# Kernel optimization log

Hardware: AMD Instinct MI355X
Metric: run time of the kernel (lower is better)

Reference implementation:

```python
import jax, jax.numpy as jnp
import numpy as np
import math

B, L, D, P = 2, 2048, 256, 32

def _lin_init(key, fan_in, shape):
    return jax.random.normal(key, shape, dtype=jnp.float32) / np.float32(math.sqrt(fan_in))

def setup_inputs() -> dict:
    key = jax.random.key(0)
    ks = jax.random.split(key, 16)
    return {
        "x": jax.random.normal(ks[0], (B, L, D), dtype=jnp.float32),
        "pos_phases": jax.random.normal(ks[1], (L, P), dtype=jnp.float32) * np.float32(math.pi),
        "w_pos_value": _lin_init(ks[2], D, (D, D)), "b_pos_value": jnp.zeros((D,), jnp.float32),
        "w_key": _lin_init(ks[3], D, (D, P)), "b_key": jnp.zeros((P,), jnp.float32),
        "w_kv": _lin_init(ks[4], D, (D, D)), "b_kv": jnp.zeros((D,), jnp.float32),
        "w_vg1": _lin_init(ks[5], 2 * D, (2 * D, D)), "b_vg1": jnp.zeros((D,), jnp.float32),
        "w_vg2": _lin_init(ks[6], D, (D, 1)), "b_vg2": jnp.zeros((1,), jnp.float32),
        "w_bg1": _lin_init(ks[7], D, (D, D // 2)), "b_bg1": jnp.zeros((D // 2,), jnp.float32),
        "w_bg2": _lin_init(ks[8], D // 2, (D // 2, 2)), "b_bg2": jnp.zeros((2,), jnp.float32),
        "ln_r_g": jnp.ones((D,), jnp.float32), "ln_r_b": jnp.zeros((D,), jnp.float32),
        "w_r1": _lin_init(ks[9], D, (D, 2 * D)), "b_r1": jnp.zeros((2 * D,), jnp.float32),
        "w_r2": _lin_init(ks[10], 2 * D, (2 * D, D)), "b_r2": jnp.zeros((D,), jnp.float32),
        "ln_o_g": jnp.ones((D,), jnp.float32), "ln_o_b": jnp.zeros((D,), jnp.float32),
        "w_out": _lin_init(ks[11], D, (D, D)), "b_out": jnp.zeros((D,), jnp.float32),
    }

def _ln(z, g, b, eps=1e-5):
    mu = z.mean(-1, keepdims=True)
    var = ((z - mu) ** 2).mean(-1, keepdims=True)
    return (z - mu) * jax.lax.rsqrt(var + eps) * g + b

def _shift1(z):
    # torch.roll(shifts=1, dims=1) then zero first position == shift right with zero pad
    return jnp.concatenate([jnp.zeros_like(z[:, :1]), z[:, :-1]], axis=1)

def reference(x, pos_phases, w_pos_value, b_pos_value, w_key, b_key, w_kv, b_kv,
              w_vg1, b_vg1, w_vg2, b_vg2, w_bg1, b_bg1, w_bg2, b_bg2,
              ln_r_g, ln_r_b, w_r1, b_r1, w_r2, b_r2, ln_o_g, ln_o_b, w_out, b_out):
    Bv, Lv, Dv = x.shape
    Pv = pos_phases.shape[1]
    inv_sqrt_p = np.float32(1.0 / math.sqrt(Pv))

    # --- positional memory ---
    pos_phasors = jnp.exp(1j * pos_phases)                      # (L,P) complex64
    pos_values = (x @ w_pos_value + b_pos_value).astype(jnp.complex64)  # (B,L,D)
    pos_bound = pos_phasors[None, :, :, None] * pos_values[:, :, None, :]  # (B,L,P,D)
    pos_memory = jnp.cumsum(pos_bound, axis=1)
    pos_query = jnp.exp(-1j * pos_phases)                       # (L,P)
    pos_retrieved = (pos_memory * pos_query[None, :, :, None]).sum(axis=2).real * inv_sqrt_p

    # --- content-based KV memory ---
    key_phases = jnp.tanh(x @ w_key + b_key) * np.float32(math.pi)  # (B,L,P)
    key_phasors = jnp.exp(1j * key_phases)
    kv_values = (x @ w_kv + b_kv).astype(jnp.complex64)         # (B,L,D)

    x_shifted = _shift1(x)
    gate_input = jnp.concatenate([x, x_shifted], axis=-1)       # (B,L,2D)
    h = jax.nn.gelu(gate_input @ w_vg1 + b_vg1, approximate=False)
    value_gates = jax.nn.sigmoid(h @ w_vg2 + b_vg2)             # (B,L,1)

    key_phasors_shifted = _shift1(key_phasors)                  # (B,L,P)
    kv_bound = (key_phasors_shifted[..., None] * kv_values[:, :, None, :]) \
               * value_gates[:, :, :, None].astype(jnp.complex64)  # (B,L,P,D)
    kv_memory = jnp.cumsum(kv_bound, axis=1)
    gate_cumsum = jnp.maximum(jnp.cumsum(value_gates, axis=1), 1.0)  # (B,L,1)
    kv_query = jnp.exp(-1j * key_phases)                        # (B,L,P)
    kv_retrieved = (kv_memory * kv_query[..., None]).sum(axis=2).real
    kv_retrieved = kv_retrieved / (jnp.sqrt(gate_cumsum) * np.float32(math.sqrt(Pv)))

    # --- blend, refine, output ---
    bg_h = jax.nn.gelu(x @ w_bg1 + b_bg1, approximate=False)
    blend = jax.nn.softmax(bg_h @ w_bg2 + b_bg2, axis=-1)       # (B,L,2)
    blended = blend[..., 0:1] * pos_retrieved + blend[..., 1:2] * kv_retrieved

    refined = jax.nn.gelu(_ln(blended, ln_r_g, ln_r_b) @ w_r1 + b_r1, approximate=False) @ w_r2 + b_r2
    return x + (_ln(refined, ln_o_g, ln_o_b) @ w_out + b_out)
```

## Files before the change

kernel.cpp:

```cpp
#include <hip/hip_runtime.h>
#include <math.h>

#define B_ 2
#define L_ 2048
#define D_ 256
#define P_ 32
#define NC_ 64
#define CL_ 32

#define INV_SQRT_P 0.17677669529663687f
#define PI_F 3.14159265358979323846f

typedef __attribute__((ext_vector_type(8))) short bf16x8;
typedef __attribute__((ext_vector_type(4))) float f32x4;

__device__ __forceinline__ float gelu_exact(float x){
    return 0.5f * x * (1.0f + erff(x * 0.70710678118654752f));
}

__device__ __forceinline__ unsigned short f2bf(float f){
    unsigned int u = __float_as_uint(f);
    u += 0x7FFFu + ((u >> 16) & 1u);
    return (unsigned short)(u >> 16);
}

__global__ __launch_bounds__(256) void k_prep(
    const float* __restrict__ pos_phases,
    const float* __restrict__ w_pv, const float* __restrict__ w_kv,
    const float* __restrict__ w_vg1, const float* __restrict__ w_bg1,
    const float* __restrict__ w_r1, const float* __restrict__ w_r2,
    const float* __restrict__ w_out, const float* __restrict__ w_key,
    unsigned short* __restrict__ wq,
    float* __restrict__ cpos, float* __restrict__ spos)
{
    int id = blockIdx.x * 256 + threadIdx.x;
    if (id < 630784){
        const float* src; int N; int local;
        if (id < 65536)       { src = w_pv;  N = 256; local = id; }
        else if (id < 131072) { src = w_kv;  N = 256; local = id - 65536; }
        else if (id < 262144) { src = w_vg1; N = 256; local = id - 131072; }
        else if (id < 294912) { src = w_bg1; N = 128; local = id - 262144; }
        else if (id < 425984) { src = w_r1;  N = 512; local = id - 294912; }
        else if (id < 557056) { src = w_r2;  N = 256; local = id - 425984; }
        else if (id < 622592) { src = w_out; N = 256; local = id - 557056; }
        else                  { src = w_key; N = 32;  local = id - 622592; }
        int j = local & 7, lane = (local >> 3) & 63, tile = local >> 9;
        int NT = N >> 4;
        int nt = tile % NT, kt = tile / NT;
        int row = kt * 32 + ((lane >> 4) << 3) + j;
        int col = nt * 16 + (lane & 15);
        wq[id] = f2bf(src[(size_t)row * N + col]);
    } else {
        int idx = id - 630784;
        float s, c;
        sincosf(pos_phases[idx], &s, &c);
        cpos[idx] = c;
        spos[idx] = s;
    }
}

__global__ __launch_bounds__(512) void k_proj(
    const float* __restrict__ x,
    const unsigned short* __restrict__ wq,
    const float* __restrict__ b_pv, const float* __restrict__ b_kv,
    const float* __restrict__ b_vg1,
    const float* __restrict__ w_vg2, const float* __restrict__ b_vg2,
    const float* __restrict__ b_bg1,
    const float* __restrict__ w_bg2, const float* __restrict__ b_bg2,
    const float* __restrict__ b_key,
    float* __restrict__ pv, float* __restrict__ kvv,
    float* __restrict__ ck, float* __restrict__ sk,
    float* __restrict__ vg, float* __restrict__ blend0, float* __restrict__ blend1)
{
    __shared__ float hbuf[16][257];
    __shared__ float bhbuf[16][129];
    __shared__ float kph[16][33];
    __shared__ float red[16][17], red2[16][17], red3[16][17];

    const int i = threadIdx.x;
    const int lane = i & 63, w = i >> 6;
    const int b = blockIdx.x >> 7, lt = blockIdx.x & 127, l0 = lt * 16;
    const int g = lane >> 4, c = lane & 15;

    bf16x8 xa[8], xs[8];
    {
        int row  = l0 + (lane & 15);
        int rowp = row - 1;
        const float* xr = x + (size_t)(b * L_ + row) * D_ + ((lane >> 4) << 3);
        #pragma unroll
        for (int kt = 0; kt < 8; ++kt){
            float4 a0 = *(const float4*)(xr + kt * 32);
            float4 a1 = *(const float4*)(xr + kt * 32 + 4);
            bf16x8 v;
            v[0] = (short)f2bf(a0.x); v[1] = (short)f2bf(a0.y);
            v[2] = (short)f2bf(a0.z); v[3] = (short)f2bf(a0.w);
            v[4] = (short)f2bf(a1.x); v[5] = (short)f2bf(a1.y);
            v[6] = (short)f2bf(a1.z); v[7] = (short)f2bf(a1.w);
            xa[kt] = v;
        }
        if (rowp >= 0){
            const float* xp = x + (size_t)(b * L_ + rowp) * D_ + ((lane >> 4) << 3);
            #pragma unroll
            for (int kt = 0; kt < 8; ++kt){
                float4 a0 = *(const float4*)(xp + kt * 32);
                float4 a1 = *(const float4*)(xp + kt * 32 + 4);
                bf16x8 v;
                v[0] = (short)f2bf(a0.x); v[1] = (short)f2bf(a0.y);
                v[2] = (short)f2bf(a0.z); v[3] = (short)f2bf(a0.w);
                v[4] = (short)f2bf(a1.x); v[5] = (short)f2bf(a1.y);
                v[6] = (short)f2bf(a1.z); v[7] = (short)f2bf(a1.w);
                xs[kt] = v;
            }
        } else {
            #pragma unroll
            for (int kt = 0; kt < 8; ++kt){
                bf16x8 v;
                #pragma unroll
                for (int j = 0; j < 8; ++j) v[j] = 0;
                xs[kt] = v;
            }
        }
    }

    const unsigned short* wpv  = wq;
    const unsigned short* wkv  = wq + 65536;
    const unsigned short* wvg1 = wq + 131072;
    const unsigned short* wbg1 = wq + 262144;
    const unsigned short* wkey = wq + 622592;

    for (int jb = w; jb < 58; jb += 8){
        f32x4 acc = {0.f, 0.f, 0.f, 0.f};
        if (jb < 2){
            int nt = jb;
            #pragma unroll
            for (int kt = 0; kt < 8; ++kt){
                bf16x8 bf = *(const bf16x8*)(wkey + (kt * 2 + nt) * 512 + lane * 8);
                acc = __builtin_amdgcn_mfma_f32_16x16x32_bf16(xa[kt], bf, acc, 0, 0, 0);
            }
            float bb = b_key[nt * 16 + c];
            #pragma unroll
            for (int r = 0; r < 4; ++r)
                kph[4 * g + r][nt * 16 + c] = acc[r] + bb;
        } else if (jb < 18){
            int nt = jb - 2;
            #pragma unroll
            for (int kt = 0; kt < 8; ++kt){
                bf16x8 bf = *(const bf16x8*)(wpv + (kt * 16 + nt) * 512 + lane * 8);
                acc = __builtin_amdgcn_mfma_f32_16x16x32_bf16(xa[kt], bf, acc, 0, 0, 0);
            }
            float bb = b_pv[nt * 16 + c];
            #pragma unroll
            for (int r = 0; r < 4; ++r)
                pv[(size_t)(b * L_ + l0 + 4 * g + r) * D_ + nt * 16 + c] = acc[r] + bb;
        } else if (jb < 34){
            int nt = jb - 18;
            #pragma unroll
            for (int kt = 0; kt < 8; ++kt){
                bf16x8 bf = *(const bf16x8*)(wkv + (kt * 16 + nt) * 512 + lane * 8);
                acc = __builtin_amdgcn_mfma_f32_16x16x32_bf16(xa[kt], bf, acc, 0, 0, 0);
            }
            float bb = b_kv[nt * 16 + c];
            #pragma unroll
            for (int r = 0; r < 4; ++r)
                kvv[(size_t)(b * L_ + l0 + 4 * g + r) * D_ + nt * 16 + c] = acc[r] + bb;
        } else if (jb < 50){
            int nt = jb - 34;
            #pragma unroll
            for (int kt = 0; kt < 8; ++kt){
                bf16x8 bf = *(const bf16x8*)(wvg1 + (kt * 16 + nt) * 512 + lane * 8);
                acc = __builtin_amdgcn_mfma_f32_16x16x32_bf16(xa[kt], bf, acc, 0, 0, 0);
            }
            #pragma unroll
            for (int kt = 8; kt < 16; ++kt){
                bf16x8 bf = *(const bf16x8*)(wvg1 + (kt * 16 + nt) * 512 + lane * 8);
                acc = __builtin_amdgcn_mfma_f32_16x16x32_bf16(xs[kt - 8], bf, acc, 0, 0, 0);
            }
            float bb = b_vg1[nt * 16 + c];
            #pragma unroll
            for (int r = 0; r < 4; ++r)
                hbuf[4 * g + r][nt * 16 + c] = gelu_exact(acc[r] + bb);
        } else {
            int nt = jb - 50;
            #pragma unroll
            for (int kt = 0; kt < 8; ++kt){
                bf16x8 bf = *(const bf16x8*)(wbg1 + (kt * 8 + nt) * 512 + lane * 8);
                acc = __builtin_amdgcn_mfma_f32_16x16x32_bf16(xa[kt], bf, acc, 0, 0, 0);
            }
            float bb = b_bg1[nt * 16 + c];
            #pragma unroll
            for (int r = 0; r < 4; ++r)
                bhbuf[4 * g + r][nt * 16 + c] = gelu_exact(acc[r] + bb);
        }
    }
    __syncthreads();

    {
        int t = i >> 5, p = i & 31;
        float a = tanhf(kph[t][p]) * PI_F;
        float s, cc;
        sincosf(a, &s, &cc);
        ck[(size_t)(b * L_ + l0 + t) * P_ + p] = cc;
        sk[(size_t)(b * L_ + l0 + t) * P_ + p] = s;
    }

    if (i < 256){
        int t = i >> 4, c2 = i & 15;
        float s = 0.f;
        #pragma unroll
        for (int m = 0; m < 16; ++m){ int dd = c2 + 16 * m; s += hbuf[t][dd] * w_vg2[dd]; }
        red[t][c2] = s;
    } else {
        int ii = i - 256;
        int t = ii >> 4, c2 = ii & 15;
        float s0 = 0.f, s1 = 0.f;
        #pragma unroll
        for (int m = 0; m < 8; ++m){
            int jj = c2 + 16 * m;
            float v = bhbuf[t][jj];
            s0 += v * w_bg2[jj * 2 + 0];
            s1 += v * w_bg2[jj * 2 + 1];
        }
        red2[t][c2] = s0; red3[t][c2] = s1;
    }
    __syncthreads();
    if (i < 16){
        float s = 0.f;
        #pragma unroll
        for (int c2 = 0; c2 < 16; ++c2) s += red[i][c2];
        s += b_vg2[0];
        vg[b * L_ + l0 + i] = 1.0f / (1.0f + expf(-s));
    } else if (i < 32){
        int t = i - 16;
        float s0 = 0.f, s1 = 0.f;
        #pragma unroll
        for (int c2 = 0; c2 < 16; ++c2){ s0 += red2[t][c2]; s1 += red3[t][c2]; }
        s0 += b_bg2[0]; s1 += b_bg2[1];
        float mx = fmaxf(s0, s1);
        float e0 = expf(s0 - mx), e1 = expf(s1 - mx);
        float inv = 1.0f / (e0 + e1);
        blend0[b * L_ + l0 + t] = e0 * inv;
        blend1[b * L_ + l0 + t] = e1 * inv;
    }
}

__global__ __launch_bounds__(256) void k_scan1(
    const float* __restrict__ cpos, const float* __restrict__ spos,
    const float* __restrict__ ck, const float* __restrict__ sk,
    const float* __restrict__ pv, const float* __restrict__ kvv,
    const float* __restrict__ vg,
    float* __restrict__ posSr, float* __restrict__ posSi,
    float* __restrict__ kvSr, float* __restrict__ kvSi,
    float* __restrict__ rnorm)
{
    const int z = blockIdx.z;
    const int c = blockIdx.x, b = blockIdx.y;
    const int i = threadIdx.x;
    if (z == 8){
        if (c != 0) return;
        float loc[8];
        float run = 0.f;
        #pragma unroll
        for (int m = 0; m < 8; ++m){ run += vg[b * L_ + i * 8 + m]; loc[m] = run; }
        __shared__ float part[256];
        part[i] = run;
        __syncthreads();
        for (int off = 1; off < 256; off <<= 1){
            float t = (i >= off) ? part[i - off] : 0.0f;
            __syncthreads();
            part[i] += t;
            __syncthreads();
        }
        float excl = part[i] - run;
        #pragma unroll
        for (int m = 0; m < 8; ++m){
            float gc = fmaxf(excl + loc[m], 1.0f);
            rnorm[b * L_ + i * 8 + m] = rsqrtf(gc) * INV_SQRT_P;
        }
        return;
    }
    const int type = z >> 2, pg = z & 3;
    const int d = i;
    const int p0 = pg * 8;
    float Sr[8], Si[8];
    #pragma unroll
    for (int j = 0; j < 8; ++j){ Sr[j] = 0.f; Si[j] = 0.f; }

    if (type == 0){
        for (int l = 0; l < CL_; ++l){
            int row = c * CL_ + l;
            float v = pv[(size_t)(b * L_ + row) * D_ + d];
            float4 c0 = *(const float4*)(cpos + row * P_ + p0);
            float4 c1 = *(const float4*)(cpos + row * P_ + p0 + 4);
            float4 s0 = *(const float4*)(spos + row * P_ + p0);
            float4 s1 = *(const float4*)(spos + row * P_ + p0 + 4);
            Sr[0] = fmaf(c0.x, v, Sr[0]); Si[0] = fmaf(s0.x, v, Si[0]);
            Sr[1] = fmaf(c0.y, v, Sr[1]); Si[1] = fmaf(s0.y, v, Si[1]);
            Sr[2] = fmaf(c0.z, v, Sr[2]); Si[2] = fmaf(s0.z, v, Si[2]);
            Sr[3] = fmaf(c0.w, v, Sr[3]); Si[3] = fmaf(s0.w, v, Si[3]);
            Sr[4] = fmaf(c1.x, v, Sr[4]); Si[4] = fmaf(s1.x, v, Si[4]);
            Sr[5] = fmaf(c1.y, v, Sr[5]); Si[5] = fmaf(s1.y, v, Si[5]);
            Sr[6] = fmaf(c1.z, v, Sr[6]); Si[6] = fmaf(s1.z, v, Si[6]);
            Sr[7] = fmaf(c1.w, v, Sr[7]); Si[7] = fmaf(s1.w, v, Si[7]);
        }
        #pragma unroll
        for (int j = 0; j < 8; ++j){
            size_t o = (size_t)((b * NC_ + c) * P_ + p0 + j) * D_ + d;
            posSr[o] = Sr[j]; posSi[o] = Si[j];
        }
    } else {
        float pc[8], ps[8];
        int srow = c * CL_ - 1;
        if (srow >= 0){
            float4 c0 = *(const float4*)(ck + ((size_t)b * L_ + srow) * P_ + p0);
            float4 c1 = *(const float4*)(ck + ((size_t)b * L_ + srow) * P_ + p0 + 4);
            float4 s0 = *(const float4*)(sk + ((size_t)b * L_ + srow) * P_ + p0);
            float4 s1 = *(const float4*)(sk + ((size_t)b * L_ + srow) * P_ + p0 + 4);
            pc[0]=c0.x; pc[1]=c0.y; pc[2]=c0.z; pc[3]=c0.w;
            pc[4]=c1.x; pc[5]=c1.y; pc[6]=c1.z; pc[7]=c1.w;
            ps[0]=s0.x; ps[1]=s0.y; ps[2]=s0.z; ps[3]=s0.w;
            ps[4]=s1.x; ps[5]=s1.y; ps[6]=s1.z; ps[7]=s1.w;
        } else {
            #pragma unroll
            for (int j = 0; j < 8; ++j){ pc[j] = 0.f; ps[j] = 0.f; }
        }
        for (int l = 0; l < CL_; ++l){
            int row = c * CL_ + l;
            float vv = kvv[(size_t)(b * L_ + row) * D_ + d] * vg[b * L_ + row];
            float4 c0 = *(const float4*)(ck + ((size_t)b * L_ + row) * P_ + p0);
            float4 c1 = *(const float4*)(ck + ((size_t)b * L_ + row) * P_ + p0 + 4);
            float4 s0 = *(const float4*)(sk + ((size_t)b * L_ + row) * P_ + p0);
            float4 s1 = *(const float4*)(sk + ((size_t)b * L_ + row) * P_ + p0 + 4);
            #pragma unroll
            for (int j = 0; j < 8; ++j){
                Sr[j] = fmaf(pc[j], vv, Sr[j]);
                Si[j] = fmaf(ps[j], vv, Si[j]);
            }
            pc[0]=c0.x; pc[1]=c0.y; pc[2]=c0.z; pc[3]=c0.w;
            pc[4]=c1.x; pc[5]=c1.y; pc[6]=c1.z; pc[7]=c1.w;
            ps[0]=s0.x; ps[1]=s0.y; ps[2]=s0.z; ps[3]=s0.w;
            ps[4]=s1.x; ps[5]=s1.y; ps[6]=s1.z; ps[7]=s1.w;
        }
        #pragma unroll
        for (int j = 0; j < 8; ++j){
            size_t o = (size_t)((b * NC_ + c) * P_ + p0 + j) * D_ + d;
            kvSr[o] = Sr[j]; kvSi[o] = Si[j];
        }
    }
}

__global__ __launch_bounds__(256) void k_prefix(
    float* __restrict__ posSr, float* __restrict__ posSi,
    float* __restrict__ kvSr, float* __restrict__ kvSi)
{
    __shared__ float4 tot_s[64][4];
    const int colLocal = threadIdx.x >> 2, seg = threadIdx.x & 3;
    const int col = blockIdx.x * 64 + colLocal;
    const int a = col >> 12;
    const int rem = col & 4095;
    const int b = rem >> 11;
    const int pd = (rem & 2047) * 4;
    float* A = (a == 0) ? posSr : (a == 1) ? posSi : (a == 2) ? kvSr : kvSi;
    float* base = A + (size_t)b * NC_ * (P_ * D_) + pd;

    float4 t[16];
    #pragma unroll
    for (int k = 0; k < 16; ++k)
        t[k] = *(const float4*)(base + (size_t)(seg * 16 + k) * (P_ * D_));
    float4 tot = {0.f, 0.f, 0.f, 0.f};
    #pragma unroll
    for (int k = 0; k < 16; ++k){
        tot.x += t[k].x; tot.y += t[k].y; tot.z += t[k].z; tot.w += t[k].w;
    }
    tot_s[colLocal][seg] = tot;
    __syncthreads();
    float4 run = {0.f, 0.f, 0.f, 0.f};
    #pragma unroll
    for (int s = 0; s < 3; ++s){
        if (s < seg){
            float4 v = tot_s[colLocal][s];
            run.x += v.x; run.y += v.y; run.z += v.z; run.w += v.w;
        }
    }
    #pragma unroll
    for (int k = 0; k < 16; ++k){
        float4 cur = t[k];
        *(float4*)(base + (size_t)(seg * 16 + k) * (P_ * D_)) = run;
        run.x += cur.x; run.y += cur.y; run.z += cur.z; run.w += cur.w;
    }
}

__global__ __launch_bounds__(256) void k_retrieve(
    const float* __restrict__ cpos, const float* __restrict__ spos,
    const float* __restrict__ ck, const float* __restrict__ sk,
    const float* __restrict__ pv, const float* __restrict__ kvv,
    const float* __restrict__ vg, const float* __restrict__ rnorm,
    const float* __restrict__ posSr, const float* __restrict__ posSi,
    const float* __restrict__ kvSr, const float* __restrict__ kvSi,
    float* __restrict__ posret, float* __restrict__ kvret)
{
    const int z = blockIdx.z;
    const int c = blockIdx.x, b = blockIdx.y;
    const int type = z >> 2, dquad = z & 3;
    const int lane = threadIdx.x & 63, wv = threadIdx.x >> 6;
    const int pg = lane >> 4, dl = lane & 15;
    const int d = dquad * 64 + wv * 16 + dl;
    const int p0 = pg * 8;

    float Sr[8], Si[8];

    if (type == 0){
        #pragma unroll
        for (int j = 0; j < 8; ++j){
            size_t o = (size_t)((b * NC_ + c) * P_ + p0 + j) * D_ + d;
            Sr[j] = posSr[o]; Si[j] = posSi[o];
        }
        for (int l = 0; l < CL_; ++l){
            int row = c * CL_ + l;
            float v = pv[(size_t)(b * L_ + row) * D_ + d];
            float4 c0 = *(const float4*)(cpos + row * P_ + p0);
            float4 c1 = *(const float4*)(cpos + row * P_ + p0 + 4);
            float4 s0 = *(const float4*)(spos + row * P_ + p0);
            float4 s1 = *(const float4*)(spos + row * P_ + p0 + 4);
            float r0 = 0.f, r1 = 0.f, r2 = 0.f, r3 = 0.f;
            Sr[0] = fmaf(c0.x, v, Sr[0]); r0 = fmaf(c0.x, Sr[0], r0);
            Si[0] = fmaf(s0.x, v, Si[0]); r1 = fmaf(s0.x, Si[0], r1);
            Sr[1] = fmaf(c0.y, v, Sr[1]); r2 = fmaf(c0.y, Sr[1], r2);
            Si[1] = fmaf(s0.y, v, Si[1]); r3 = fmaf(s0.y, Si[1], r3);
            Sr[2] = fmaf(c0.z, v, Sr[2]); r0 = fmaf(c0.z, Sr[2], r0);
            Si[2] = fmaf(s0.z, v, Si[2]); r1 = fmaf(s0.z, Si[2], r1);
            Sr[3] = fmaf(c0.w, v, Sr[3]); r2 = fmaf(c0.w, Sr[3], r2);
            Si[3] = fmaf(s0.w, v, Si[3]); r3 = fmaf(s0.w, Si[3], r3);
            Sr[4] = fmaf(c1.x, v, Sr[4]); r0 = fmaf(c1.x, Sr[4], r0);
            Si[4] = fmaf(s1.x, v, Si[4]); r1 = fmaf(s1.x, Si[4], r1);
            Sr[5] = fmaf(c1.y, v, Sr[5]); r2 = fmaf(c1.y, Sr[5], r2);
            Si[5] = fmaf(s1.y, v, Si[5]); r3 = fmaf(s1.y, Si[5], r3);
            Sr[6] = fmaf(c1.z, v, Sr[6]); r0 = fmaf(c1.z, Sr[6], r0);
            Si[6] = fmaf(s1.z, v, Si[6]); r1 = fmaf(s1.z, Si[6], r1);
            Sr[7] = fmaf(c1.w, v, Sr[7]); r2 = fmaf(c1.w, Sr[7], r2);
            Si[7] = fmaf(s1.w, v, Si[7]); r3 = fmaf(s1.w, Si[7], r3);
            float r = (r0 + r1) + (r2 + r3);
            r += __shfl_xor(r, 16, 64);
            r += __shfl_xor(r, 32, 64);
            if (pg == 0)
                posret[(size_t)(b * L_ + row) * D_ + d] = r * INV_SQRT_P;
        }
    } else {
        #pragma unroll
        for (int j = 0; j < 8; ++j){
            size_t o = (size_t)((b * NC_ + c) * P_ + p0 + j) * D_ + d;
            Sr[j] = kvSr[o]; Si[j] = kvSi[o];
        }
        float pc[8], ps[8];
        int srow = c * CL_ - 1;
        if (srow >= 0){
            float4 c0 = *(const float4*)(ck + ((size_t)b * L_ + srow) * P_ + p0);
            float4 c1 = *(const float4*)(ck + ((size_t)b * L_ + srow) * P_ + p0 + 4);
            float4 s0 = *(const float4*)(sk + ((size_t)b * L_ + srow) * P_ + p0);
            float4 s1 = *(const float4*)(sk + ((size_t)b * L_ + srow) * P_ + p0 + 4);
            pc[0]=c0.x; pc[1]=c0.y; pc[2]=c0.z; pc[3]=c0.w;
            pc[4]=c1.x; pc[5]=c1.y; pc[6]=c1.z; pc[7]=c1.w;
            ps[0]=s0.x; ps[1]=s0.y; ps[2]=s0.z; ps[3]=s0.w;
            ps[4]=s1.x; ps[5]=s1.y; ps[6]=s1.z; ps[7]=s1.w;
        } else {
            #pragma unroll
            for (int j = 0; j < 8; ++j){ pc[j] = 0.f; ps[j] = 0.f; }
        }
        for (int l = 0; l < CL_; ++l){
            int row = c * CL_ + l;
            float vv = kvv[(size_t)(b * L_ + row) * D_ + d] * vg[b * L_ + row];
            float rn = rnorm[b * L_ + row];
            float4 c0 = *(const float4*)(ck + ((size_t)b * L_ + row) * P_ + p0);
            float4 c1 = *(const float4*)(ck + ((size_t)b * L_ + row) * P_ + p0 + 4);
            float4 s0 = *(const float4*)(sk + ((size_t)b * L_ + row) * P_ + p0);
            float4 s1 = *(const float4*)(sk + ((size_t)b * L_ + row) * P_ + p0 + 4);
            float qc[8], qs[8];
            qc[0]=c0.x; qc[1]=c0.y; qc[2]=c0.z; qc[3]=c0.w;
            qc[4]=c1.x; qc[5]=c1.y; qc[6]=c1.z; qc[7]=c1.w;
            qs[0]=s0.x; qs[1]=s0.y; qs[2]=s0.z; qs[3]=s0.w;
            qs[4]=s1.x; qs[5]=s1.y; qs[6]=s1.z; qs[7]=s1.w;
            float r0 = 0.f, r1 = 0.f, r2 = 0.f, r3 = 0.f;
            #pragma unroll
            for (int j = 0; j < 8; ++j){
                Sr[j] = fmaf(pc[j], vv, Sr[j]);
                Si[j] = fmaf(ps[j], vv, Si[j]);
                if (j & 1){ r2 = fmaf(qc[j], Sr[j], r2); r3 = fmaf(qs[j], Si[j], r3); }
                else      { r0 = fmaf(qc[j], Sr[j], r0); r1 = fmaf(qs[j], Si[j], r1); }
                pc[j] = qc[j]; ps[j] = qs[j];
            }
            float r = (r0 + r1) + (r2 + r3);
            r += __shfl_xor(r, 16, 64);
            r += __shfl_xor(r, 32, 64);
            if (pg == 0)
                kvret[(size_t)(b * L_ + row) * D_ + d] = r * rn;
        }
    }
}

__global__ __launch_bounds__(512) void k_final(
    const float* __restrict__ x,
    const float* __restrict__ posret, const float* __restrict__ kvret,
    const float* __restrict__ blend0, const float* __restrict__ blend1,
    const unsigned short* __restrict__ wq,
    const float* __restrict__ ln_r_g, const float* __restrict__ ln_r_b,
    const float* __restrict__ b_r1, const float* __restrict__ b_r2,
    const float* __restrict__ ln_o_g, const float* __restrict__ ln_o_b,
    const float* __restrict__ b_out,
    float* __restrict__ out)
{
    __shared__ float zbuf[16][257];
    __shared__ __align__(16) unsigned short aA[8][512];
    __shared__ __align__(16) unsigned short aH[16][512];
    __shared__ float red[16][17], red2[16][17];
    __shared__ float mu[16], rs[16];

    const int i = threadIdx.x, lane = i & 63, w = i >> 6;
    const int b = blockIdx.x >> 7, l0 = (blockIdx.x & 127) * 16;
    const int g = lane >> 4, c = lane & 15;
    const unsigned short* wr1  = wq + 294912;
    const unsigned short* wr2  = wq + 425984;
    const unsigned short* wout = wq + 557056;

    {
        int t = i >> 5, c0 = (i & 31) * 8;
        size_t base = (size_t)(b * L_ + l0 + t) * D_ + c0;
        float w0 = blend0[b * L_ + l0 + t], w1 = blend1[b * L_ + l0 + t];
        #pragma unroll
        for (int m = 0; m < 8; ++m)
            zbuf[t][c0 + m] = w0 * posret[base + m] + w1 * kvret[base + m];
    }
    __syncthreads();

    if (i < 256){
        int t = i >> 4, c2 = i & 15;
        float s = 0.f, s2 = 0.f;
        #pragma unroll
        for (int m = 0; m < 16; ++m){ float v = zbuf[t][c2 + 16 * m]; s += v; s2 += v * v; }
        red[t][c2] = s; red2[t][c2] = s2;
    }
    __syncthreads();
    if (i < 16){
        float s = 0.f, s2 = 0.f;
        #pragma unroll
        for (int c2 = 0; c2 < 16; ++c2){ s += red[i][c2]; s2 += red2[i][c2]; }
        float mean = s * (1.0f / 256.0f);
        float var  = s2 * (1.0f / 256.0f) - mean * mean;
        mu[i] = mean; rs[i] = rsqrtf(var + 1e-5f);
    }
    __syncthreads();

    {
        int kt = i >> 6;
        int t2 = lane & 15, kb = kt * 32 + ((lane >> 4) << 3);
        float m_ = mu[t2], r_ = rs[t2];
        bf16x8 v8;
        #pragma unroll
        for (int j = 0; j < 8; ++j){
            int k = kb + j;
            float v = (zbuf[t2][k] - m_) * r_ * ln_r_g[k] + ln_r_b[k];
            v8[j] = (short)f2bf(v);
        }
        *(bf16x8*)&aA[kt][lane * 8] = v8;
    }
    __syncthreads();

    {
        bf16x8 afr[8];
        #pragma unroll
        for (int kt = 0; kt < 8; ++kt) afr[kt] = *(const bf16x8*)&aA[kt][lane * 8];
        for (int q = 0; q < 4; ++q){
            int nt = w + 8 * q;
            f32x4 acc = {0.f, 0.f, 0.f, 0.f};
            #pragma unroll
            for (int kt = 0; kt < 8; ++kt){
                bf16x8 bf = *(const bf16x8*)(wr1 + (kt * 32 + nt) * 512 + lane * 8);
                acc = __builtin_amdgcn_mfma_f32_16x16x32_bf16(afr[kt], bf, acc, 0, 0, 0);
            }
            float bb = b_r1[nt * 16 + c];
            #pragma unroll
            for (int r = 0; r < 4; ++r){
                float hv = gelu_exact(acc[r] + bb);
                int t = 4 * g + r, hcol = nt * 16 + c;
                int kt2 = hcol >> 5, kk = hcol & 31;
                int lane2 = ((kk >> 3) << 4) + t, j2 = kk & 7;
                aH[kt2][lane2 * 8 + j2] = f2bf(hv);
            }
        }
    }
    __syncthreads();

    {
        bf16x8 hfr[16];
        #pragma unroll
        for (int kt = 0; kt < 16; ++kt) hfr[kt] = *(const bf16x8*)&aH[kt][lane * 8];
        for (int q = 0; q < 2; ++q){
            int nt = w + 8 * q;
            f32x4 acc = {0.f, 0.f, 0.f, 0.f};
            #pragma unroll
            for (int kt = 0; kt < 16; ++kt){
                bf16x8 bf = *(const bf16x8*)(wr2 + (kt * 16 + nt) * 512 + lane * 8);
                acc = __builtin_amdgcn_mfma_f32_16x16x32_bf16(hfr[kt], bf, acc, 0, 0, 0);
            }
            float bb = b_r2[nt * 16 + c];
            #pragma unroll
            for (int r = 0; r < 4; ++r)
                zbuf[4 * g + r][nt * 16 + c] = acc[r] + bb;
        }
    }
    __syncthreads();

    if (i < 256){
        int t = i >> 4, c2 = i & 15;
        float s = 0.f, s2 = 0.f;
        #pragma unroll
        for (int m = 0; m < 16; ++m){ float v = zbuf[t][c2 + 16 * m]; s += v; s2 += v * v; }
        red[t][c2] = s; red2[t][c2] = s2;
    }
    __syncthreads();
    if (i < 16){
        float s = 0.f, s2 = 0.f;
        #pragma unroll
        for (int c2 = 0; c2 < 16; ++c2){ s += red[i][c2]; s2 += red2[i][c2]; }
        float mean = s * (1.0f / 256.0f);
        float var  = s2 * (1.0f / 256.0f) - mean * mean;
        mu[i] = mean; rs[i] = rsqrtf(var + 1e-5f);
    }
    __syncthreads();

    {
        int kt = i >> 6;
        int t2 = lane & 15, kb = kt * 32 + ((lane >> 4) << 3);
        float m_ = mu[t2], r_ = rs[t2];
        bf16x8 v8;
        #pragma unroll
        for (int j = 0; j < 8; ++j){
            int k = kb + j;
            float v = (zbuf[t2][k] - m_) * r_ * ln_o_g[k] + ln_o_b[k];
            v8[j] = (short)f2bf(v);
        }
        *(bf16x8*)&aA[kt][lane * 8] = v8;
    }
    __syncthreads();

    {
        bf16x8 azr[8];
        #pragma unroll
        for (int kt = 0; kt < 8; ++kt) azr[kt] = *(const bf16x8*)&aA[kt][lane * 8];
        for (int q = 0; q < 2; ++q){
            int nt = w + 8 * q;
            f32x4 acc = {0.f, 0.f, 0.f, 0.f};
            #pragma unroll
            for (int kt = 0; kt < 8; ++kt){
                bf16x8 bf = *(const bf16x8*)(wout + (kt * 16 + nt) * 512 + lane * 8);
                acc = __builtin_amdgcn_mfma_f32_16x16x32_bf16(azr[kt], bf, acc, 0, 0, 0);
            }
            float bb = b_out[nt * 16 + c];
            #pragma unroll
            for (int r = 0; r < 4; ++r){
                size_t o = (size_t)(b * L_ + l0 + 4 * g + r) * D_ + nt * 16 + c;
                out[o] = x[o] + acc[r] + bb;
            }
        }
    }
}

extern "C" void kernel_launch(void* const* d_in, const int* in_sizes, int n_in,
                              void* d_out, int out_size, void* d_ws, size_t ws_size,
                              hipStream_t stream) {
    const float* x          = (const float*)d_in[0];
    const float* pos_phases = (const float*)d_in[1];
    const float* w_pv       = (const float*)d_in[2];
    const float* b_pv       = (const float*)d_in[3];
    const float* w_key      = (const float*)d_in[4];
    const float* b_key      = (const float*)d_in[5];
    const float* w_kv       = (const float*)d_in[6];
    const float* b_kv       = (const float*)d_in[7];
    const float* w_vg1      = (const float*)d_in[8];
    const float* b_vg1      = (const float*)d_in[9];
    const float* w_vg2      = (const float*)d_in[10];
    const float* b_vg2      = (const float*)d_in[11];
    const float* w_bg1      = (const float*)d_in[12];
    const float* b_bg1      = (const float*)d_in[13];
    const float* w_bg2      = (const float*)d_in[14];
    const float* b_bg2      = (const float*)d_in[15];
    const float* ln_r_g     = (const float*)d_in[16];
    const float* ln_r_b     = (const float*)d_in[17];
    const float* w_r1       = (const float*)d_in[18];
    const float* b_r1       = (const float*)d_in[19];
    const float* w_r2       = (const float*)d_in[20];
    const float* b_r2       = (const float*)d_in[21];
    const float* ln_o_g     = (const float*)d_in[22];
    const float* ln_o_b     = (const float*)d_in[23];
    const float* w_out      = (const float*)d_in[24];
    const float* b_out      = (const float*)d_in[25];
    float* out = (float*)d_out;

    float* ws = (float*)d_ws;
    size_t off = 0;
    float* cpos   = ws + off; off += (size_t)L_ * P_;
    float* spos   = ws + off; off += (size_t)L_ * P_;
    float* pv     = ws + off; off += (size_t)B_ * L_ * D_;
    float* kvv    = ws + off; off += (size_t)B_ * L_ * D_;
    float* ck     = ws + off; off += (size_t)B_ * L_ * P_;
    float* sk     = ws + off; off += (size_t)B_ * L_ * P_;
    float* vg     = ws + off; off += (size_t)B_ * L_;
    float* rnorm  = ws + off; off += (size_t)B_ * L_;
    float* blend0 = ws + off; off += (size_t)B_ * L_;
    float* blend1 = ws + off; off += (size_t)B_ * L_;
    float* posret = ws + off; off += (size_t)B_ * L_ * D_;
    float* kvret  = ws + off; off += (size_t)B_ * L_ * D_;
    float* posSr  = ws + off; off += (size_t)B_ * NC_ * P_ * D_;
    float* posSi  = ws + off; off += (size_t)B_ * NC_ * P_ * D_;
    float* kvSr   = ws + off; off += (size_t)B_ * NC_ * P_ * D_;
    float* kvSi   = ws + off; off += (size_t)B_ * NC_ * P_ * D_;
    unsigned short* wq = (unsigned short*)(ws + off); off += 630784 / 2;

    k_prep<<<2720, 256, 0, stream>>>(pos_phases,
        w_pv, w_kv, w_vg1, w_bg1, w_r1, w_r2, w_out, w_key,
        wq, cpos, spos);

    k_proj<<<B_ * 128, 512, 0, stream>>>(x, wq,
        b_pv, b_kv, b_vg1, w_vg2, b_vg2, b_bg1, w_bg2, b_bg2, b_key,
        pv, kvv, ck, sk, vg, blend0, blend1);

    k_scan1<<<dim3(NC_, B_, 9), 256, 0, stream>>>(cpos, spos, ck, sk, pv, kvv, vg,
                                                  posSr, posSi, kvSr, kvSi, rnorm);

    k_prefix<<<256, 256, 0, stream>>>(posSr, posSi, kvSr, kvSi);

    k_retrieve<<<dim3(NC_, B_, 8), 256, 0, stream>>>(cpos, spos, ck, sk, pv, kvv,
                                                     vg, rnorm,
                                                     posSr, posSi, kvSr, kvSi,
                                                     posret, kvret);

    k_final<<<B_ * 128, 512, 0, stream>>>(x, posret, kvret, blend0, blend1, wq,
        ln_r_g, ln_r_b, b_r1, b_r2, ln_o_g, ln_o_b, b_out, out);
}
```

Baseline: 89.07 us.

## Store intermediates as bf16, prefold value gate, halve chunk count

The pos/kv value projections and retrieved outputs now pass through global memory as bf16 instead of fp32, roughly halving that intermediate traffic. The kv value is multiplied by the value gate inside the projection kernel before it is stored, so the scan and retrieve kernels no longer read vg. The chunk count drops from 64 to 32 with longer chunks, which halves the chunk-state buffers and the prefix work but gives fewer blocks and longer serial loops per block. The price is bf16 rounding on intermediates and lower parallelism in the scan and retrieve kernels.

```diff
diff --git a/kernel.cpp b/kernel.cpp
--- a/kernel.cpp
+++ b/kernel.cpp
@@ -5,8 +5,8 @@
 #define L_ 2048
 #define D_ 256
 #define P_ 32
-#define NC_ 64
-#define CL_ 32
+#define NC_ 32
+#define CL_ 64
 
 #define INV_SQRT_P 0.17677669529663687f
 #define PI_F 3.14159265358979323846f
@@ -22,6 +22,10 @@
     unsigned int u = __float_as_uint(f);
     u += 0x7FFFu + ((u >> 16) & 1u);
     return (unsigned short)(u >> 16);
+}
+
+__device__ __forceinline__ float bf2f(unsigned short u){
+    return __uint_as_float(((unsigned int)u) << 16);
 }
 
 __global__ __launch_bounds__(256) void k_prep(
@@ -68,14 +72,16 @@
     const float* __restrict__ b_bg1,
     const float* __restrict__ w_bg2, const float* __restrict__ b_bg2,
     const float* __restrict__ b_key,
-    float* __restrict__ pv, float* __restrict__ kvv,
+    unsigned short* __restrict__ pvb, unsigned short* __restrict__ kvvb,
     float* __restrict__ ck, float* __restrict__ sk,
     float* __restrict__ vg, float* __restrict__ blend0, float* __restrict__ blend1)
 {
     __shared__ float hbuf[16][257];
+    __shared__ float kvbuf[16][257];
     __shared__ float bhbuf[16][129];
     __shared__ float kph[16][33];
     __shared__ float red[16][17], red2[16][17], red3[16][17];
+    __shared__ float vgs[16];
 
     const int i = threadIdx.x;
     const int lane = i & 63, w = i >> 6;
@@ -151,7 +157,7 @@
             float bb = b_pv[nt * 16 + c];
             #pragma unroll
             for (int r = 0; r < 4; ++r)
-                pv[(size_t)(b * L_ + l0 + 4 * g + r) * D_ + nt * 16 + c] = acc[r] + bb;
+                pvb[(size_t)(b * L_ + l0 + 4 * g + r) * D_ + nt * 16 + c] = f2bf(acc[r] + bb);
         } else if (jb < 34){
             int nt = jb - 18;
             #pragma unroll
@@ -162,7 +168,7 @@
             float bb = b_kv[nt * 16 + c];
             #pragma unroll
             for (int r = 0; r < 4; ++r)
-                kvv[(size_t)(b * L_ + l0 + 4 * g + r) * D_ + nt * 16 + c] = acc[r] + bb;
+                kvbuf[4 * g + r][nt * 16 + c] = acc[r] + bb;
         } else if (jb < 50){
             int nt = jb - 34;
             #pragma unroll
@@ -228,7 +234,9 @@
         #pragma unroll
         for (int c2 = 0; c2 < 16; ++c2) s += red[i][c2];
         s += b_vg2[0];
-        vg[b * L_ + l0 + i] = 1.0f / (1.0f + expf(-s));
+        float gv = 1.0f / (1.0f + expf(-s));
+        vg[b * L_ + l0 + i] = gv;
+        vgs[i] = gv;
     } else if (i < 32){
         int t = i - 16;
         float s0 = 0.f, s1 = 0.f;
@@ -241,12 +249,22 @@
         blend0[b * L_ + l0 + t] = e0 * inv;
         blend1[b * L_ + l0 + t] = e1 * inv;
     }
+    __syncthreads();
+
+    {
+        int d = i & 255, tg = i >> 8;
+        #pragma unroll
+        for (int m = 0; m < 8; ++m){
+            int tok = tg * 8 + m;
+            kvvb[(size_t)(b * L_ + l0 + tok) * D_ + d] = f2bf(kvbuf[tok][d] * vgs[tok]);
+        }
+    }
 }
 
 __global__ __launch_bounds__(256) void k_scan1(
     const float* __restrict__ cpos, const float* __restrict__ spos,
     const float* __restrict__ ck, const float* __restrict__ sk,
-    const float* __restrict__ pv, const float* __restrict__ kvv,
+    const unsigned short* __restrict__ pvb, const unsigned short* __restrict__ kvvb,
     const float* __restrict__ vg,
     float* __restrict__ posSr, float* __restrict__ posSi,
     float* __restrict__ kvSr, float* __restrict__ kvSi,
@@ -288,7 +306,7 @@
     if (type == 0){
         for (int l = 0; l < CL_; ++l){
             int row = c * CL_ + l;
-            float v = pv[(size_t)(b * L_ + row) * D_ + d];
+            float v = bf2f(pvb[(size_t)(b * L_ + row) * D_ + d]);
             float4 c0 = *(const float4*)(cpos + row * P_ + p0);
             float4 c1 = *(const float4*)(cpos + row * P_ + p0 + 4);
             float4 s0 = *(const float4*)(spos + row * P_ + p0);
@@ -325,7 +343,7 @@
         }
         for (int l = 0; l < CL_; ++l){
             int row = c * CL_ + l;
-            float vv = kvv[(size_t)(b * L_ + row) * D_ + d] * vg[b * L_ + row];
+            float vv = bf2f(kvvb[(size_t)(b * L_ + row) * D_ + d]);
             float4 c0 = *(const float4*)(ck + ((size_t)b * L_ + row) * P_ + p0);
             float4 c1 = *(const float4*)(ck + ((size_t)b * L_ + row) * P_ + p0 + 4);
             float4 s0 = *(const float4*)(sk + ((size_t)b * L_ + row) * P_ + p0);
@@ -362,13 +380,13 @@
     float* A = (a == 0) ? posSr : (a == 1) ? posSi : (a == 2) ? kvSr : kvSi;
     float* base = A + (size_t)b * NC_ * (P_ * D_) + pd;
 
-    float4 t[16];
+    float4 t[8];
     #pragma unroll
-    for (int k = 0; k < 16; ++k)
-        t[k] = *(const float4*)(base + (size_t)(seg * 16 + k) * (P_ * D_));
+    for (int k = 0; k < 8; ++k)
+        t[k] = *(const float4*)(base + (size_t)(seg * 8 + k) * (P_ * D_));
     float4 tot = {0.f, 0.f, 0.f, 0.f};
     #pragma unroll
-    for (int k = 0; k < 16; ++k){
+    for (int k = 0; k < 8; ++k){
         tot.x += t[k].x; tot.y += t[k].y; tot.z += t[k].z; tot.w += t[k].w;
     }
     tot_s[colLocal][seg] = tot;
@@ -382,9 +400,9 @@
         }
     }
     #pragma unroll
-    for (int k = 0; k < 16; ++k){
+    for (int k = 0; k < 8; ++k){
         float4 cur = t[k];
-        *(float4*)(base + (size_t)(seg * 16 + k) * (P_ * D_)) = run;
+        *(float4*)(base + (size_t)(seg * 8 + k) * (P_ * D_)) = run;
         run.x += cur.x; run.y += cur.y; run.z += cur.z; run.w += cur.w;
     }
 }
@@ -392,11 +410,11 @@
 __global__ __launch_bounds__(256) void k_retrieve(
     const float* __restrict__ cpos, const float* __restrict__ spos,
     const float* __restrict__ ck, const float* __restrict__ sk,
-    const float* __restrict__ pv, const float* __restrict__ kvv,
-    const float* __restrict__ vg, const float* __restrict__ rnorm,
+    const unsigned short* __restrict__ pvb, const unsigned short* __restrict__ kvvb,
+    const float* __restrict__ rnorm,
     const float* __restrict__ posSr, const float* __restrict__ posSi,
     const float* __restrict__ kvSr, const float* __restrict__ kvSi,
-    float* __restrict__ posret, float* __restrict__ kvret)
+    unsigned short* __restrict__ posretb, unsigned short* __restrict__ kvretb)
 {
     const int z = blockIdx.z;
     const int c = blockIdx.x, b = blockIdx.y;
@@ -416,7 +434,7 @@
         }
         for (int l = 0; l < CL_; ++l){
             int row = c * CL_ + l;
-            float v = pv[(size_t)(b * L_ + row) * D_ + d];
+            float v = bf2f(pvb[(size_t)(b * L_ + row) * D_ + d]);
             float4 c0 = *(const float4*)(cpos + row * P_ + p0);
             float4 c1 = *(const float4*)(cpos + row * P_ + p0 + 4);
             float4 s0 = *(const float4*)(spos + row * P_ + p0);
@@ -442,7 +460,7 @@
             r += __shfl_xor(r, 16, 64);
             r += __shfl_xor(r, 32, 64);
             if (pg == 0)
-                posret[(size_t)(b * L_ + row) * D_ + d] = r * INV_SQRT_P;
+                posretb[(size_t)(b * L_ + row) * D_ + d] = f2bf(r * INV_SQRT_P);
         }
     } else {
         #pragma unroll
@@ -467,7 +485,7 @@
         }
         for (int l = 0; l < CL_; ++l){
             int row = c * CL_ + l;
-            float vv = kvv[(size_t)(b * L_ + row) * D_ + d] * vg[b * L_ + row];
+            float vv = bf2f(kvvb[(size_t)(b * L_ + row) * D_ + d]);
             float rn = rnorm[b * L_ + row];
             float4 c0 = *(const float4*)(ck + ((size_t)b * L_ + row) * P_ + p0);
             float4 c1 = *(const float4*)(ck + ((size_t)b * L_ + row) * P_ + p0 + 4);
@@ -491,14 +509,14 @@
             r += __shfl_xor(r, 16, 64);
             r += __shfl_xor(r, 32, 64);
             if (pg == 0)
-                kvret[(size_t)(b * L_ + row) * D_ + d] = r * rn;
+                kvretb[(size_t)(b * L_ + row) * D_ + d] = f2bf(r * rn);
         }
     }
 }
 
 __global__ __launch_bounds__(512) void k_final(
     const float* __restrict__ x,
-    const float* __restrict__ posret, const float* __restrict__ kvret,
+    const unsigned short* __restrict__ posretb, const unsigned short* __restrict__ kvretb,
     const float* __restrict__ blend0, const float* __restrict__ blend1,
     const unsigned short* __restrict__ wq,
     const float* __restrict__ ln_r_g, const float* __restrict__ ln_r_b,
@@ -524,9 +542,12 @@
         int t = i >> 5, c0 = (i & 31) * 8;
         size_t base = (size_t)(b * L_ + l0 + t) * D_ + c0;
         float w0 = blend0[b * L_ + l0 + t], w1 = blend1[b * L_ + l0 + t];
+        bf16x8 pp = *(const bf16x8*)(posretb + base);
+        bf16x8 kk = *(const bf16x8*)(kvretb + base);
         #pragma unroll
         for (int m = 0; m < 8; ++m)
-            zbuf[t][c0 + m] = w0 * posret[base + m] + w1 * kvret[base + m];
+            zbuf[t][c0 + m] = w0 * bf2f((unsigned short)pp[m])
+                            + w1 * bf2f((unsigned short)kk[m]);
     }
     __syncthreads();
 
@@ -698,21 +719,21 @@
     size_t off = 0;
     float* cpos   = ws + off; off += (size_t)L_ * P_;
     float* spos   = ws + off; off += (size_t)L_ * P_;
-    float* pv     = ws + off; off += (size_t)B_ * L_ * D_;
-    float* kvv    = ws + off; off += (size_t)B_ * L_ * D_;
     float* ck     = ws + off; off += (size_t)B_ * L_ * P_;
     float* sk     = ws + off; off += (size_t)B_ * L_ * P_;
     float* vg     = ws + off; off += (size_t)B_ * L_;
     float* rnorm  = ws + off; off += (size_t)B_ * L_;
     float* blend0 = ws + off; off += (size_t)B_ * L_;
     float* blend1 = ws + off; off += (size_t)B_ * L_;
-    float* posret = ws + off; off += (size_t)B_ * L_ * D_;
-    float* kvret  = ws + off; off += (size_t)B_ * L_ * D_;
     float* posSr  = ws + off; off += (size_t)B_ * NC_ * P_ * D_;
     float* posSi  = ws + off; off += (size_t)B_ * NC_ * P_ * D_;
     float* kvSr   = ws + off; off += (size_t)B_ * NC_ * P_ * D_;
     float* kvSi   = ws + off; off += (size_t)B_ * NC_ * P_ * D_;
-    unsigned short* wq = (unsigned short*)(ws + off); off += 630784 / 2;
+    unsigned short* wq      = (unsigned short*)(ws + off); off += 630784 / 2;
+    unsigned short* pvb     = (unsigned short*)(ws + off); off += (size_t)B_ * L_ * D_ / 2;
+    unsigned short* kvvb    = (unsigned short*)(ws + off); off += (size_t)B_ * L_ * D_ / 2;
+    unsigned short* posretb = (unsigned short*)(ws + off); off += (size_t)B_ * L_ * D_ / 2;
+    unsigned short* kvretb  = (unsigned short*)(ws + off); off += (size_t)B_ * L_ * D_ / 2;
 
     k_prep<<<2720, 256, 0, stream>>>(pos_phases,
         w_pv, w_kv, w_vg1, w_bg1, w_r1, w_r2, w_out, w_key,
@@ -720,18 +741,18 @@
 
     k_proj<<<B_ * 128, 512, 0, stream>>>(x, wq,
         b_pv, b_kv, b_vg1, w_vg2, b_vg2, b_bg1, w_bg2, b_bg2, b_key,
-        pv, kvv, ck, sk, vg, blend0, blend1);
-
-    k_scan1<<<dim3(NC_, B_, 9), 256, 0, stream>>>(cpos, spos, ck, sk, pv, kvv, vg,
+        pvb, kvvb, ck, sk, vg, blend0, blend1);
+
+    k_scan1<<<dim3(NC_, B_, 9), 256, 0, stream>>>(cpos, spos, ck, sk, pvb, kvvb, vg,
                                                   posSr, posSi, kvSr, kvSi, rnorm);
 
     k_prefix<<<256, 256, 0, stream>>>(posSr, posSi, kvSr, kvSi);
 
-    k_retrieve<<<dim3(NC_, B_, 8), 256, 0, stream>>>(cpos, spos, ck, sk, pv, kvv,
-                                                     vg, rnorm,
+    k_retrieve<<<dim3(NC_, B_, 8), 256, 0, stream>>>(cpos, spos, ck, sk, pvb, kvvb,
+                                                     rnorm,
                                                      posSr, posSi, kvSr, kvSi,
-                                                     posret, kvret);
-
-    k_final<<<B_ * 128, 512, 0, stream>>>(x, posret, kvret, blend0, blend1, wq,
+                                                     posretb, kvretb);
+
+    k_final<<<B_ * 128, 512, 0, stream>>>(x, posretb, kvretb, blend0, blend1, wq,
         ln_r_g, ln_r_b, b_r1, b_r2, ln_o_g, ln_o_b, b_out, out);
 }
```

Result: slower. 103.5 us (+16.2%).
